# Kernel optimization log

Hardware: AMD Instinct MI355X
Metric: run time of the kernel (lower is better)

Reference implementation:

```python
import jax, jax.numpy as jnp
import numpy as np

IOU_THRESH = 0.5


def _iou_xcycwh(a, b):
    # a: (A,4) center-format anchors, b: (M,4) center-format gt boxes -> (A,M)
    ax1, ay1 = a[:, 0] - a[:, 2] * 0.5, a[:, 1] - a[:, 3] * 0.5
    ax2, ay2 = a[:, 0] + a[:, 2] * 0.5, a[:, 1] + a[:, 3] * 0.5
    bx1, by1 = b[:, 0] - b[:, 2] * 0.5, b[:, 1] - b[:, 3] * 0.5
    bx2, by2 = b[:, 0] + b[:, 2] * 0.5, b[:, 1] + b[:, 3] * 0.5
    iw = jnp.clip(jnp.minimum(ax2[:, None], bx2[None, :]) - jnp.maximum(ax1[:, None], bx1[None, :]), 0.0)
    ih = jnp.clip(jnp.minimum(ay2[:, None], by2[None, :]) - jnp.maximum(ay1[:, None], by1[None, :]), 0.0)
    inter = iw * ih
    area_a = (a[:, 2] * a[:, 3])[:, None]
    area_b = (b[:, 2] * b[:, 3])[None, :]
    return inter / (area_a + area_b - inter)


def _per_image(cls_pred, reg_pred, ann, anchors, num_classes):
    # cls_pred: (A,C) probs in (0,1); reg_pred: (A,5); ann: (M,5) [x,y,w,h,cls]; anchors: (A,4)
    dt = cls_pred.dtype
    valid = ann[:, 4] != -1
    # top-left -> center (matches in-place += w/2, h/2 in torch)
    boxes = jnp.stack([ann[:, 0] + ann[:, 2] * 0.5, ann[:, 1] + ann[:, 3] * 0.5, ann[:, 2], ann[:, 3]], axis=-1)
    ious = _iou_xcycwh(anchors, boxes)                       # (A,M)
    ious = jnp.where(valid[None, :], ious, -jnp.inf)
    ious_max = ious.max(axis=1)
    ious_argmax = ious.argmax(axis=1)
    pos = ious_max >= IOU_THRESH                             # (A,)
    posf = pos.astype(dt)
    npos = pos.sum()
    denom = jnp.maximum(npos, 1).astype(dt)                  # clamp(num_positive_anchors, min=1)
    assigned = jnp.concatenate([boxes, ann[:, 4:5]], axis=-1)[ious_argmax]  # (A,5)
    gt_cls = jax.nn.one_hot(assigned[:, 4].astype(jnp.int32), num_classes, dtype=dt) * posf[:, None]
    bce = -(gt_cls * jnp.log(cls_pred) + (1.0 - gt_cls) * jnp.log(1.0 - cls_pred))
    cls_loss = (bce * posf[:, None]).sum() / denom
    gt_w = jnp.maximum(assigned[:, 2], 1.0)
    gt_h = jnp.maximum(assigned[:, 3], 1.0)
    sig_tx_gt = jax.nn.sigmoid(assigned[:, 0] - anchors[:, 0])
    sig_ty_gt = jax.nn.sigmoid(assigned[:, 1] - anchors[:, 1])
    tw_gt = jnp.log(gt_w / anchors[:, 2])
    th_gt = jnp.log(gt_h / anchors[:, 3])

    def mse(p, t):  # MSELoss over positive anchors = masked sum / npos
        return (posf * (p - t) ** 2).sum() / denom

    reg = (mse(jax.nn.sigmoid(reg_pred[:, 0]), sig_tx_gt)
           + mse(jax.nn.sigmoid(reg_pred[:, 1]), sig_ty_gt)
           + mse(reg_pred[:, 2], tw_gt)
           + mse(reg_pred[:, 3], th_gt)
           + mse(reg_pred[:, 4], jnp.ones_like(reg_pred[:, 4])))
    reg_loss = jnp.where(npos > 0, reg / denom, jnp.zeros((), dt))
    has_valid = valid.any()
    cls_loss = jnp.where(has_valid, cls_loss, jnp.zeros((), dt))
    return cls_loss, reg_loss


def reference(predictions, bbox_annotations, anchors, input_dim, num_classes, num_anchors, grid_size):
    B = predictions.shape[0]
    cls = predictions[..., 5:].reshape(B, -1, num_classes)   # (B,A,C)
    reg = predictions[..., :5].reshape(B, -1, 5)             # (B,A,5)
    anc = anchors.reshape(-1, 4)                             # (A,4)
    cls_l, reg_l = jax.vmap(lambda c, r, a: _per_image(c, r, a, anc, num_classes))(cls, reg, bbox_annotations)
    return cls_l.mean(keepdims=True), reg_l.mean(keepdims=True)


def setup_inputs() -> dict:
    key = jax.random.key(0)
    k1, k2, k3, k4 = jax.random.split(key, 4)
    B, NA, G, C, M, INPUT = 16, 3, 76, 80, 32, 608
    stride = INPUT / G
    # predictions: probabilities/pre-sigmoid values in (0.01, 0.99) (raw log requires p in (0,1))
    u = jax.random.uniform(k1, (B, NA, G, G, C + 5), dtype=jnp.float32)
    predictions = 0.01 + 0.98 * u
    # anchors: grid-cell centers in pixels + 3 per-cell anchor sizes
    xs = (jnp.arange(G, dtype=jnp.float32) + 0.5) * stride
    cyg, cxg = jnp.meshgrid(xs, xs, indexing='ij')
    sizes = jnp.array([[12.0, 16.0], [24.0, 32.0], [48.0, 40.0]], dtype=jnp.float32)
    anchors = jnp.stack([
        jnp.broadcast_to(cxg, (NA, G, G)),
        jnp.broadcast_to(cyg, (NA, G, G)),
        jnp.broadcast_to(sizes[:, 0][:, None, None], (NA, G, G)),
        jnp.broadcast_to(sizes[:, 1][:, None, None], (NA, G, G))], axis=-1)
    # annotations: top-left x,y + w,h in pixels + class id; last 8 boxes padded with cls=-1
    wh = jax.random.uniform(k2, (B, M, 2), minval=8.0, maxval=64.0)
    xy = jax.random.uniform(k3, (B, M, 2), minval=0.0, maxval=INPUT - 64.0)
    cls_id = jax.random.randint(k4, (B, M, 1), 0, C).astype(jnp.float32)
    valid = (jnp.arange(M) < 24)[None, :, None]
    ann = jnp.concatenate([xy, wh, jnp.where(valid, cls_id, -1.0)], axis=-1)
    return {"predictions": predictions, "bbox_annotations": ann, "anchors": anchors,
            "input_dim": INPUT, "num_classes": C, "num_anchors": NA, "grid_size": G}
```

## Files before the change

kernel.cpp:

```cpp
#include <hip/hip_runtime.h>
#include <math.h>


#define NCLS 85
#define CVAL 80

__device__ __forceinline__ float sigm(float x) {
    return 1.0f / (1.0f + expf(-x));
}

__global__ void __launch_bounds__(256)
yolo_match_kernel(const float* __restrict__ pred,
                  const float* __restrict__ ann,
                  const float* __restrict__ anc,
                  float* __restrict__ acc,
                  int A, int M)
{
    const int b = blockIdx.y;
    const int a = blockIdx.x * blockDim.x + threadIdx.x;

    __shared__ float s_bx1[64], s_by1[64], s_bx2[64], s_by2[64];
    __shared__ float s_bcx[64], s_bcy[64], s_bw[64], s_bh[64], s_area[64];
    __shared__ int   s_cls[64];

    if (threadIdx.x < (unsigned)M) {
        const int m = threadIdx.x;
        const float* r = ann + ((long long)b * M + m) * 5;
        const float x = r[0], y = r[1], w = r[2], h = r[3], c = r[4];
        const float cx = x + 0.5f * w;
        const float cy = y + 0.5f * h;
        s_bcx[m] = cx; s_bcy[m] = cy; s_bw[m] = w; s_bh[m] = h;
        s_bx1[m] = cx - 0.5f * w; s_by1[m] = cy - 0.5f * h;
        s_bx2[m] = cx + 0.5f * w; s_by2[m] = cy + 0.5f * h;
        s_area[m] = w * h;
        s_cls[m] = (c != -1.0f) ? (int)c : -1;
    }
    __syncthreads();

    if (a >= A) return;

    const float4 av = ((const float4*)anc)[a];
    const float acx = av.x, acy = av.y, aw = av.z, ah = av.w;
    const float ax1 = acx - 0.5f * aw, ay1 = acy - 0.5f * ah;
    const float ax2 = acx + 0.5f * aw, ay2 = acy + 0.5f * ah;
    const float aarea = aw * ah;

    float best = -INFINITY;
    int bm = 0;
    for (int m = 0; m < M; ++m) {
        float iw = fminf(ax2, s_bx2[m]) - fmaxf(ax1, s_bx1[m]);
        float ih = fminf(ay2, s_by2[m]) - fmaxf(ay1, s_by1[m]);
        iw = fmaxf(iw, 0.0f);
        ih = fmaxf(ih, 0.0f);
        const float inter = iw * ih;
        float iou = inter / (aarea + s_area[m] - inter);
        if (s_cls[m] < 0) iou = -INFINITY;
        if (iou > best) { best = iou; bm = m; }
    }

    if (!(best >= 0.5f)) return;

    const float bcx = s_bcx[bm], bcy = s_bcy[bm];
    const float bw = s_bw[bm], bh = s_bh[bm];
    const int k = s_cls[bm];

    const float* row = pred + ((long long)b * A + a) * NCLS;

    const float r0 = row[0], r1 = row[1], r2 = row[2], r3 = row[3], r4 = row[4];
    const float e0 = sigm(r0) - sigm(bcx - acx);
    const float e1 = sigm(r1) - sigm(bcy - acy);
    const float e2 = r2 - logf(fmaxf(bw, 1.0f) / aw);
    const float e3 = r3 - logf(fmaxf(bh, 1.0f) / ah);
    const float e4 = r4 - 1.0f;
    const float reg_sq = e0*e0 + e1*e1 + e2*e2 + e3*e3 + e4*e4;

    float cls_sum = 0.0f;
    for (int c = 0; c < CVAL; ++c) {
        const float p = row[5 + c];
        cls_sum += (c == k) ? -logf(p) : -logf(1.0f - p);
    }

    atomicAdd(&acc[b * 3 + 0], cls_sum);
    atomicAdd(&acc[b * 3 + 1], reg_sq);
    atomicAdd(&acc[b * 3 + 2], 1.0f);
}

__global__ void yolo_finalize_kernel(const float* __restrict__ acc,
                                     float* __restrict__ out, int B)
{
    if (blockIdx.x == 0 && threadIdx.x == 0) {
        float cs = 0.0f, rs = 0.0f;
        for (int b = 0; b < B; ++b) {
            const float npos = acc[b * 3 + 2];
            const float denom = fmaxf(npos, 1.0f);
            cs += acc[b * 3 + 0] / denom;
            rs += (npos > 0.0f) ? acc[b * 3 + 1] / (denom * denom) : 0.0f;
        }
        out[0] = cs / (float)B;
        out[1] = rs / (float)B;
    }
}

extern "C" void kernel_launch(void* const* d_in, const int* in_sizes, int n_in,
                              void* d_out, int out_size, void* d_ws, size_t ws_size,
                              hipStream_t stream) {
    const float* pred = (const float*)d_in[0];
    const float* ann  = (const float*)d_in[1];
    const float* anc  = (const float*)d_in[2];
    float* out = (float*)d_out;

    const int A = in_sizes[2] / 4;
    const int B = in_sizes[0] / (A * NCLS);
    const int M = in_sizes[1] / (5 * B);

    float* acc = (float*)d_ws;
    hipMemsetAsync(acc, 0, (size_t)B * 3 * sizeof(float), stream);

    dim3 block(256);
    dim3 grid((A + 255) / 256, B);
    yolo_match_kernel<<<grid, block, 0, stream>>>(pred, ann, anc, acc, A, M);
    yolo_finalize_kernel<<<1, 64, 0, stream>>>(acc, out, B);
}
```

Before: 157.4 us.

## Replace global atomics with per-block partial sums and parallel finalize

Each block now reduces its thread results with wave shuffles and shared memory, then writes one per-block partial triple instead of every positive anchor issuing three global atomicAdds. The finalize kernel reduces the partials with 16 threads per image, which removes the memset launch. The aim is to cut atomic contention on a few addresses and drop one launch. In exchange, every block now runs a reduction even when it has no positives, and the finalize kernel assumes B is at most 16.

```diff
diff --git a/kernel.cpp b/kernel.cpp
--- a/kernel.cpp
+++ b/kernel.cpp
@@ -4,20 +4,21 @@
 
 #define NCLS 85
 #define CVAL 80
+#define BLK  256
 
 __device__ __forceinline__ float sigm(float x) {
     return 1.0f / (1.0f + expf(-x));
 }
 
-__global__ void __launch_bounds__(256)
+__global__ void __launch_bounds__(BLK)
 yolo_match_kernel(const float* __restrict__ pred,
                   const float* __restrict__ ann,
                   const float* __restrict__ anc,
-                  float* __restrict__ acc,
+                  float* __restrict__ partial,
                   int A, int M)
 {
     const int b = blockIdx.y;
-    const int a = blockIdx.x * blockDim.x + threadIdx.x;
+    const int a = blockIdx.x * BLK + threadIdx.x;
 
     __shared__ float s_bx1[64], s_by1[64], s_bx2[64], s_by2[64];
     __shared__ float s_bcx[64], s_bcy[64], s_bw[64], s_bh[64], s_area[64];
@@ -37,65 +38,102 @@
     }
     __syncthreads();
 
-    if (a >= A) return;
+    float cls_sum = 0.0f, reg_sq = 0.0f, np = 0.0f;
 
-    const float4 av = ((const float4*)anc)[a];
-    const float acx = av.x, acy = av.y, aw = av.z, ah = av.w;
-    const float ax1 = acx - 0.5f * aw, ay1 = acy - 0.5f * ah;
-    const float ax2 = acx + 0.5f * aw, ay2 = acy + 0.5f * ah;
-    const float aarea = aw * ah;
+    if (a < A) {
+        const float4 av = ((const float4*)anc)[a];
+        const float acx = av.x, acy = av.y, aw = av.z, ah = av.w;
+        const float ax1 = acx - 0.5f * aw, ay1 = acy - 0.5f * ah;
+        const float ax2 = acx + 0.5f * aw, ay2 = acy + 0.5f * ah;
+        const float aarea = aw * ah;
 
-    float best = -INFINITY;
-    int bm = 0;
-    for (int m = 0; m < M; ++m) {
-        float iw = fminf(ax2, s_bx2[m]) - fmaxf(ax1, s_bx1[m]);
-        float ih = fminf(ay2, s_by2[m]) - fmaxf(ay1, s_by1[m]);
-        iw = fmaxf(iw, 0.0f);
-        ih = fmaxf(ih, 0.0f);
-        const float inter = iw * ih;
-        float iou = inter / (aarea + s_area[m] - inter);
-        if (s_cls[m] < 0) iou = -INFINITY;
-        if (iou > best) { best = iou; bm = m; }
+        float best = -INFINITY;
+        int bm = 0;
+        for (int m = 0; m < M; ++m) {
+            float iw = fminf(ax2, s_bx2[m]) - fmaxf(ax1, s_bx1[m]);
+            float ih = fminf(ay2, s_by2[m]) - fmaxf(ay1, s_by1[m]);
+            iw = fmaxf(iw, 0.0f);
+            ih = fmaxf(ih, 0.0f);
+            const float inter = iw * ih;
+            float iou = inter / (aarea + s_area[m] - inter);
+            if (s_cls[m] < 0) iou = -INFINITY;
+            if (iou > best) { best = iou; bm = m; }
+        }
+
+        if (best >= 0.5f) {
+            np = 1.0f;
+            const float bcx = s_bcx[bm], bcy = s_bcy[bm];
+            const float bw = s_bw[bm], bh = s_bh[bm];
+            const int k = s_cls[bm];
+
+            const float* row = pred + ((long long)b * A + a) * NCLS;
+
+            const float r0 = row[0], r1 = row[1], r2 = row[2], r3 = row[3], r4 = row[4];
+            const float e0 = sigm(r0) - sigm(bcx - acx);
+            const float e1 = sigm(r1) - sigm(bcy - acy);
+            const float e2 = r2 - logf(fmaxf(bw, 1.0f) / aw);
+            const float e3 = r3 - logf(fmaxf(bh, 1.0f) / ah);
+            const float e4 = r4 - 1.0f;
+            reg_sq = e0*e0 + e1*e1 + e2*e2 + e3*e3 + e4*e4;
+
+            for (int c = 0; c < CVAL; ++c) {
+                const float p = row[5 + c];
+                cls_sum += (c == k) ? -logf(p) : -logf(1.0f - p);
+            }
+        }
     }
 
-    if (!(best >= 0.5f)) return;
-
-    const float bcx = s_bcx[bm], bcy = s_bcy[bm];
-    const float bw = s_bw[bm], bh = s_bh[bm];
-    const int k = s_cls[bm];
-
-    const float* row = pred + ((long long)b * A + a) * NCLS;
-
-    const float r0 = row[0], r1 = row[1], r2 = row[2], r3 = row[3], r4 = row[4];
-    const float e0 = sigm(r0) - sigm(bcx - acx);
-    const float e1 = sigm(r1) - sigm(bcy - acy);
-    const float e2 = r2 - logf(fmaxf(bw, 1.0f) / aw);
-    const float e3 = r3 - logf(fmaxf(bh, 1.0f) / ah);
-    const float e4 = r4 - 1.0f;
-    const float reg_sq = e0*e0 + e1*e1 + e2*e2 + e3*e3 + e4*e4;
-
-    float cls_sum = 0.0f;
-    for (int c = 0; c < CVAL; ++c) {
-        const float p = row[5 + c];
-        cls_sum += (c == k) ? -logf(p) : -logf(1.0f - p);
+    for (int off = 32; off > 0; off >>= 1) {
+        cls_sum += __shfl_down(cls_sum, off);
+        reg_sq  += __shfl_down(reg_sq,  off);
+        np      += __shfl_down(np,      off);
     }
-
-    atomicAdd(&acc[b * 3 + 0], cls_sum);
-    atomicAdd(&acc[b * 3 + 1], reg_sq);
-    atomicAdd(&acc[b * 3 + 2], 1.0f);
+    __shared__ float s_red[4][3];
+    const int wave = threadIdx.x >> 6;
+    const int lane = threadIdx.x & 63;
+    if (lane == 0) {
+        s_red[wave][0] = cls_sum;
+        s_red[wave][1] = reg_sq;
+        s_red[wave][2] = np;
+    }
+    __syncthreads();
+    if (threadIdx.x == 0) {
+        float c = 0.0f, r = 0.0f, n = 0.0f;
+        for (int w = 0; w < 4; ++w) { c += s_red[w][0]; r += s_red[w][1]; n += s_red[w][2]; }
+        float* dst = partial + ((long long)b * gridDim.x + blockIdx.x) * 3;
+        dst[0] = c; dst[1] = r; dst[2] = n;
+    }
 }
 
-__global__ void yolo_finalize_kernel(const float* __restrict__ acc,
-                                     float* __restrict__ out, int B)
+__global__ void __launch_bounds__(256)
+yolo_finalize_kernel(const float* __restrict__ partial,
+                     float* __restrict__ out, int B, int P)
 {
-    if (blockIdx.x == 0 && threadIdx.x == 0) {
+    const int t = threadIdx.x;
+    const int b = t >> 4;
+    const int j = t & 15;
+    float c = 0.0f, r = 0.0f, n = 0.0f;
+    if (b < B) {
+        for (int p = j; p < P; p += 16) {
+            const float* s = partial + ((long long)b * P + p) * 3;
+            c += s[0]; r += s[1]; n += s[2];
+        }
+    }
+    for (int m = 8; m > 0; m >>= 1) {
+        c += __shfl_xor(c, m);
+        r += __shfl_xor(r, m);
+        n += __shfl_xor(n, m);
+    }
+    __shared__ float s_c[16], s_r[16];
+    if (j == 0 && b < B) {
+        const float denom = fmaxf(n, 1.0f);
+        s_c[b] = c / denom;
+        s_r[b] = (n > 0.0f) ? r / (denom * denom) : 0.0f;
+    }
+    __syncthreads();
+    if (t == 0) {
         float cs = 0.0f, rs = 0.0f;
-        for (int b = 0; b < B; ++b) {
-            const float npos = acc[b * 3 + 2];
-            const float denom = fmaxf(npos, 1.0f);
-            cs += acc[b * 3 + 0] / denom;
-            rs += (npos > 0.0f) ? acc[b * 3 + 1] / (denom * denom) : 0.0f;
-        }
+        for (int i = 0; i < B; ++i) { cs += s_c[i]; rs += s_r[i]; }
         out[0] = cs / (float)B;
         out[1] = rs / (float)B;
     }
@@ -112,12 +150,11 @@
     const int A = in_sizes[2] / 4;
     const int B = in_sizes[0] / (A * NCLS);
     const int M = in_sizes[1] / (5 * B);
+    const int P = (A + BLK - 1) / BLK;
 
-    float* acc = (float*)d_ws;
-    hipMemsetAsync(acc, 0, (size_t)B * 3 * sizeof(float), stream);
+    float* partial = (float*)d_ws;
 
-    dim3 block(256);
-    dim3 grid((A + 255) / 256, B);
-    yolo_match_kernel<<<grid, block, 0, stream>>>(pred, ann, anc, acc, A, M);
-    yolo_finalize_kernel<<<1, 64, 0, stream>>>(acc, out, B);
+    dim3 grid(P, B);
+    yolo_match_kernel<<<grid, dim3(BLK), 0, stream>>>(pred, ann, anc, partial, A, M);
+    yolo_finalize_kernel<<<1, 256, 0, stream>>>(partial, out, B, P);
 }
```

Result: faster. 146.1 us, median of 2 (-7.2%).
